# Optimization experiments

Hardware: AMD Instinct MI355X
Metric: run time of the kernel (lower is better)

## Reference

```python
import jax, jax.numpy as jnp
import numpy as np

# Module config (matches init_kwargs attn_neighborhood_size=[7,7])
KH, KW = 7, 7
B, N_HEADS, HEIGHT, WIDTH, D = 2, 8, 48, 48, 64


def setup_inputs() -> dict:
    key = jax.random.key(0)
    x = jax.random.normal(key, (B, N_HEADS, HEIGHT * WIDTH, D), dtype=jnp.float32)
    return {"x": x, "height": HEIGHT, "width": WIDTH}


def reference(x, height, width):
    """LocalExpansion forward.

    The torch module runs conv2d with KH*KW one-hot impulse filters and
    padding='same'. Filter (i, j) with pad = (K-1)//2 produces
    out[y, x] = in[y + i - ph, x + j - pw] with zero fill at boundaries,
    i.e. a padded shifted gather (im2col/unfold). We implement that directly.

    x: [b, h, N, d] with N = height * width
    returns: [b, h, N, KH*KW, d]
    """
    b, h, n, d = x.shape
    img = x.reshape(b, h, height, width, d)  # [b, h, H, W, d]
    ph, pw = (KH - 1) // 2, (KW - 1) // 2  # 'same' padding for odd kernels
    xp = jnp.pad(img, ((0, 0), (0, 0), (ph, ph), (pw, pw), (0, 0)))
    # Filter index c = i * KW + j -> shifted slice (i outer, j inner),
    # matching the torch impulse-filter ordering.
    shifts = [
        xp[:, :, i:i + height, j:j + width, :]
        for i in range(KH) for j in range(KW)
    ]
    y = jnp.stack(shifts, axis=4)  # [b, h, H, W, K, d]
    return y.reshape(b, h, height * width, KH * KW, d)
```

## Files before the change

### kernel.cpp

```cpp
#include <hip/hip_runtime.h>


#define KH 7
#define KW 7
#define HEIGHT 48
#define WIDTH 48
#define DDIM 64
#define NPIX (HEIGHT * WIDTH)
#define KK (KH * KW)
#define UNROLL 4
#define NXCD 8

typedef __attribute__((ext_vector_type(4))) float nt_float4;

__global__ __launch_bounds__(256) void local_expansion_kernel(
    const float* __restrict__ in, float* __restrict__ out) {
    int cpx = gridDim.x >> 3;
    int bid = (blockIdx.x & (NXCD - 1)) * cpx + (blockIdx.x >> 3);
    int base4 = bid * (256 * UNROLL) + threadIdx.x;

    nt_float4 v[UNROLL];

#pragma unroll
    for (int u = 0; u < UNROLL; ++u) {
        int idx4 = base4 + u * 256;

        int d4   = idx4 & 15;
        int rem  = idx4 >> 4;
        int c    = rem % KK;
        int rem2 = rem / KK;
        int n    = rem2 % NPIX;
        int bh   = rem2 / NPIX;

        int y = n / WIDTH;
        int x = n - y * WIDTH;
        int i = c / KW;
        int j = c - i * KW;

        int sy = y + i - (KH - 1) / 2;
        int sx = x + j - (KW - 1) / 2;

        bool inb = ((unsigned)sy < (unsigned)HEIGHT) & ((unsigned)sx < (unsigned)WIDTH);

        int syc = min(max(sy, 0), HEIGHT - 1);
        int sxc = min(max(sx, 0), WIDTH - 1);
        int in4 = (bh * NPIX + syc * WIDTH + sxc) * (DDIM / 4) + d4;

        nt_float4 t = ((const nt_float4*)in)[in4];
        nt_float4 z = (nt_float4)(0.f);
        v[u] = inb ? t : z;
    }

#pragma unroll
    for (int u = 0; u < UNROLL; ++u) {
        __builtin_nontemporal_store(v[u], ((nt_float4*)out) + base4 + u * 256);
    }
}

extern "C" void kernel_launch(void* const* d_in, const int* in_sizes, int n_in,
                              void* d_out, int out_size, void* d_ws, size_t ws_size,
                              hipStream_t stream) {
    const float* x = (const float*)d_in[0];
    float* out = (float*)d_out;

    int total4 = out_size / 4;
    int blocks = total4 / (256 * UNROLL);
    local_expansion_kernel<<<dim3(blocks), 256, 0, stream>>>(x, out);
}
```

Baseline: 463.9 us.

## Stage input halo tile in LDS and emit neighborhood outputs from shared memory

Each block now handles a 16-pixel row segment and loads its 7x22 input halo into LDS once. Outputs are then written by reading the shifted neighbors from LDS instead of issuing redundant global gathers. This removes repeated global/cache loads and per-element div/mod decomposition, at the cost of a block-wide barrier and LDS capacity limiting occupancy.

New measurement: 467.8 us. No clear change (+0.8%).

```diff
diff --git a/kernel.cpp b/kernel.cpp
--- a/kernel.cpp
+++ b/kernel.cpp
@@ -6,54 +6,66 @@
 #define HEIGHT 48
 #define WIDTH 48
 #define DDIM 64
+#define D4 (DDIM / 4)
 #define NPIX (HEIGHT * WIDTH)
 #define KK (KH * KW)
-#define UNROLL 4
+#define PX 16
+#define HALO ((KH - 1) / 2)
+#define LW (PX + 2 * HALO)
 #define NXCD 8
 
 typedef __attribute__((ext_vector_type(4))) float nt_float4;
 
 __global__ __launch_bounds__(256) void local_expansion_kernel(
     const float* __restrict__ in, float* __restrict__ out) {
+
+    __shared__ nt_float4 lds[KH * LW * D4];
+
     int cpx = gridDim.x >> 3;
     int bid = (blockIdx.x & (NXCD - 1)) * cpx + (blockIdx.x >> 3);
-    int base4 = bid * (256 * UNROLL) + threadIdx.x;
 
-    nt_float4 v[UNROLL];
+    int t   = threadIdx.x;
+    int bh  = bid / (HEIGHT * (WIDTH / PX));
+    int rem = bid - bh * (HEIGHT * (WIDTH / PX));
+    int y   = rem / (WIDTH / PX);
+    int x0  = (rem - y * (WIDTH / PX)) * PX;
 
-#pragma unroll
-    for (int u = 0; u < UNROLL; ++u) {
-        int idx4 = base4 + u * 256;
+    const nt_float4* inp = (const nt_float4*)in + bh * (NPIX * D4);
 
-        int d4   = idx4 & 15;
-        int rem  = idx4 >> 4;
-        int c    = rem % KK;
-        int rem2 = rem / KK;
-        int n    = rem2 % NPIX;
-        int bh   = rem2 / NPIX;
+    for (int s = t; s < KH * LW * D4; s += 256) {
+        int d4 = s & (D4 - 1);
+        int p  = s >> 4;
+        int r  = p / LW;
+        int lx = p - r * LW;
+        int ra = y - HALO + r;
+        int ca = x0 - HALO + lx;
+        if (((unsigned)ra < (unsigned)HEIGHT) & ((unsigned)ca < (unsigned)WIDTH)) {
+            lds[s] = inp[(ra * WIDTH + ca) * D4 + d4];
+        }
+    }
+    __syncthreads();
 
-        int y = n / WIDTH;
-        int x = n - y * WIDTH;
-        int i = c / KW;
-        int j = c - i * KW;
+    nt_float4* op = (nt_float4*)out +
+                    (size_t)(bh * NPIX + y * WIDTH + x0) * (KK * D4);
 
-        int sy = y + i - (KH - 1) / 2;
-        int sx = x + j - (KW - 1) / 2;
+    int d4 = t & (D4 - 1);
+    int th = t >> 4;
+    nt_float4 z = (nt_float4)(0.f);
 
-        bool inb = ((unsigned)sy < (unsigned)HEIGHT) & ((unsigned)sx < (unsigned)WIDTH);
-
-        int syc = min(max(sy, 0), HEIGHT - 1);
-        int sxc = min(max(sx, 0), WIDTH - 1);
-        int in4 = (bh * NPIX + syc * WIDTH + sxc) * (DDIM / 4) + d4;
-
-        nt_float4 t = ((const nt_float4*)in)[in4];
-        nt_float4 z = (nt_float4)(0.f);
-        v[u] = inb ? t : z;
-    }
-
-#pragma unroll
-    for (int u = 0; u < UNROLL; ++u) {
-        __builtin_nontemporal_store(v[u], ((nt_float4*)out) + base4 + u * 256);
+#pragma unroll 7
+    for (int k = 0; k < KK; ++k) {
+        int o  = k * 256 + t;
+        int rm = k * 16 + th;
+        int xi = rm / KK;
+        int c  = rm - xi * KK;
+        int i  = c / KW;
+        int j  = c - i * KW;
+        int sy  = y + i - HALO;
+        int sxa = x0 + xi + j - HALO;
+        bool inb = ((unsigned)sy < (unsigned)HEIGHT) &
+                   ((unsigned)sxa < (unsigned)WIDTH);
+        nt_float4 v = lds[(i * LW + xi + j) * D4 + d4];
+        __builtin_nontemporal_store(inb ? v : z, op + o);
     }
 }
 
@@ -64,6 +76,6 @@
     float* out = (float*)d_out;
 
     int total4 = out_size / 4;
-    int blocks = total4 / (256 * UNROLL);
+    int blocks = total4 / (KK * D4 * PX);
     local_expansion_kernel<<<dim3(blocks), 256, 0, stream>>>(x, out);
 }
```
